# Optimization experiments

Hardware: AMD Instinct MI355X
Metric: run time of the kernel (lower is better)

Reference implementation:

```python
import jax, jax.numpy as jnp
import numpy as np

D_MODEL = 512
PROJ = 2 * D_MODEL  # 1024
N_STATES = 32
KSIZE = 4
LN_EPS = 1e-3  # keras LayerNormalization default epsilon


def setup_inputs() -> dict:
    key = jax.random.key(0)
    ks = jax.random.split(key, 16)
    B, L = 2, 2048
    s_in = 1.0 / np.sqrt(D_MODEL)
    s_pr = 1.0 / np.sqrt(PROJ)
    x = jax.random.normal(ks[0], (B, L, D_MODEL), dtype=jnp.float32)
    # LayerNorm params
    ln_gamma = jnp.ones((D_MODEL,), jnp.float32)
    ln_beta = jnp.zeros((D_MODEL,), jnp.float32)
    # dense1 / dense2: d_model -> proj
    W1 = jax.random.normal(ks[1], (D_MODEL, PROJ), jnp.float32) * s_in
    b1 = jnp.zeros((PROJ,), jnp.float32)
    W2 = jax.random.normal(ks[2], (D_MODEL, PROJ), jnp.float32) * s_in
    b2 = jnp.zeros((PROJ,), jnp.float32)
    # depthwise causal conv1d: kernel (K, 1, PROJ) in WIO layout, groups=PROJ
    conv_k = jax.random.normal(ks[3], (KSIZE, 1, PROJ), jnp.float32) * 0.5
    conv_b = jnp.zeros((PROJ,), jnp.float32)
    # SSM params
    A_log = jnp.log(jnp.broadcast_to(jnp.arange(1, N_STATES + 1, dtype=jnp.float32), (PROJ, N_STATES)))
    D_skip = jnp.ones((PROJ,), jnp.float32)
    WB = jax.random.normal(ks[4], (PROJ, N_STATES), jnp.float32) * s_pr
    bB = jnp.zeros((N_STATES,), jnp.float32)
    WC = jax.random.normal(ks[5], (PROJ, N_STATES), jnp.float32) * s_pr
    bC = jnp.zeros((N_STATES,), jnp.float32)
    Wd = jax.random.normal(ks[6], (PROJ, PROJ), jnp.float32) * s_pr
    bd = jnp.zeros((PROJ,), jnp.float32)
    # dense3: proj -> d_model
    W3 = jax.random.normal(ks[7], (PROJ, D_MODEL), jnp.float32) * s_pr
    b3 = jnp.zeros((D_MODEL,), jnp.float32)
    return dict(x=x, ln_gamma=ln_gamma, ln_beta=ln_beta, W1=W1, b1=b1, W2=W2, b2=b2,
                conv_k=conv_k, conv_b=conv_b, A_log=A_log, D_skip=D_skip,
                WB=WB, bB=bB, WC=WC, bC=bC, Wd=Wd, bd=bd, W3=W3, b3=b3)


def _layernorm(x, gamma, beta):
    mu = jnp.mean(x, axis=-1, keepdims=True)
    var = jnp.mean(jnp.square(x - mu), axis=-1, keepdims=True)
    return (x - mu) * jax.lax.rsqrt(var + LN_EPS) * gamma + beta


def _causal_dwconv(x, k, b):
    # x: [B,L,C], k: [K,1,C], depthwise causal conv (left-pad K-1)
    y = jax.lax.conv_general_dilated(
        x, k, window_strides=(1,), padding=[(KSIZE - 1, 0)],
        dimension_numbers=('NWC', 'WIO', 'NWC'), feature_group_count=PROJ)
    return y + b


def _selective_scan(u, delta, A, Bm, Cm, D_skip):
    # u, delta: [B,L,D]; A: [D,N]; Bm, Cm: [B,L,N]; D_skip: [D]
    deltaA = jnp.einsum('bld,dn->bldn', delta, A)                 # [B,L,D,N]
    deltaBu = jnp.einsum('bld,bld,bln->bldn', delta, u, Bm)        # [B,L,D,N]
    # shift deltaA left by one along L, zero at the end (pad trick in source)
    shifted = jnp.concatenate([deltaA[:, 1:], jnp.zeros_like(deltaA[:, :1])], axis=1)
    # reversed cumsum along L, then exp
    e = jnp.exp(jnp.flip(jnp.cumsum(jnp.flip(shifted, axis=1), axis=1), axis=1))
    xs = jnp.cumsum(deltaBu * e, axis=1) / (e + 1e-12)
    y = jnp.einsum('bldn,bln->bld', xs, Cm)
    return y + u * D_skip


def reference(x, ln_gamma, ln_beta, W1, b1, W2, b2, conv_k, conv_b,
              A_log, D_skip, WB, bB, WC, bC, Wd, bd, W3, b3):
    h = _layernorm(x, ln_gamma, ln_beta)
    x1 = h @ W1 + b1                      # [B,L,PROJ]
    x1 = _causal_dwconv(x1, conv_k, conv_b)
    x1 = jax.nn.silu(x1)
    A = -jnp.exp(A_log)                    # [PROJ,N]
    Cm = x1 @ WC + bC                      # [B,L,N]
    Bm = x1 @ WB + bB                      # [B,L,N]
    delta = jax.nn.softplus(x1 @ Wd + bd)  # [B,L,PROJ]
    y = _selective_scan(x1, delta, A, Bm, Cm, D_skip)
    x2 = jax.nn.silu(h @ W2 + b2)
    out = (y * x2) @ W3 + b3 + x           # residual; dropout is identity at inference
    return out
```

## Files before the change

kernel.cpp:

```cpp
#include <hip/hip_runtime.h>
#include <stdint.h>

#define L_SEQ 2048
#define BATCH 2
#define DMODEL 512
#define PROJ 1024
#define NST 32
#define NCATU 1088
#define ROWS (BATCH*L_SEQ)
#define THRESH 50.0f

typedef float f32x4 __attribute__((ext_vector_type(4)));
typedef short short8 __attribute__((ext_vector_type(8)));

__device__ inline float bf2f(unsigned short u){ uint32_t x=((uint32_t)u)<<16; float f; __builtin_memcpy(&f,&x,4); return f; }
__device__ inline unsigned short f2bf(float f){ uint32_t x; __builtin_memcpy(&x,&f,4); uint32_t r=x+0x7FFFu+((x>>16)&1u); return (unsigned short)(r>>16); }
__device__ inline float siluf(float x){ return x/(1.f+__expf(-x)); }
__device__ inline float softplusf(float x){ return x>20.f? x : log1pf(__expf(x)); }

#define AS1(p) ((const __attribute__((address_space(1))) void*)(p))
#define AS3(p) ((__attribute__((address_space(3))) void*)(p))

template<int N> __device__ inline void wait_vmcnt(){
  if constexpr (N==0)      asm volatile("s_waitcnt vmcnt(0)" ::: "memory");
  else if constexpr (N==2) asm volatile("s_waitcnt vmcnt(2)" ::: "memory");
  else if constexpr (N==4) asm volatile("s_waitcnt vmcnt(4)" ::: "memory");
  else if constexpr (N==6) asm volatile("s_waitcnt vmcnt(6)" ::: "memory");
  else                     asm volatile("s_waitcnt vmcnt(8)" ::: "memory");
}

__global__ __launch_bounds__(256)
void prep_kernel(const float* __restrict__ W1, const float* __restrict__ b1,
                 const float* __restrict__ W2, const float* __restrict__ b2,
                 const float* __restrict__ Wd, const float* __restrict__ bd,
                 const float* __restrict__ WB, const float* __restrict__ bB,
                 const float* __restrict__ WC, const float* __restrict__ bC,
                 const float* __restrict__ W3,
                 unsigned short* __restrict__ W12t, unsigned short* __restrict__ Wcatt,
                 unsigned short* __restrict__ W3t, float* __restrict__ bias12,
                 float* __restrict__ biascat)
{
  int i = blockIdx.x*256 + threadIdx.x;
  const int nA = 2048*512;
  const int nB = NCATU*1024;
  const int nC = 512*1024;
  if (i < nA) {
    int n = i >> 9, k = i & 511;
    float v = (n < 1024) ? W1[k*1024 + n] : W2[k*1024 + (n-1024)];
    W12t[i] = f2bf(v);
    return;
  }
  i -= nA;
  if (i < nB) {
    int n = i >> 10, k = i & 1023;
    float v;
    if (n < 1024) v = Wd[k*1024 + n];
    else if (n < 1056) v = WB[k*32 + (n-1024)];
    else v = WC[k*32 + (n-1056)];
    Wcatt[i] = f2bf(v);
    return;
  }
  i -= nB;
  if (i < nC) {
    int n = i >> 10, k = i & 1023;
    W3t[i] = f2bf(W3[k*512 + n]);
    return;
  }
  i -= nC;
  if (i < 2048) { bias12[i] = (i < 1024) ? b1[i] : b2[i-1024]; return; }
  i -= 2048;
  if (i < NCATU) {
    biascat[i] = (i < 1024) ? bd[i] : (i < 1056) ? bB[i-1024] : bC[i-1056];
  }
}

__global__ __launch_bounds__(256)
void ln_kernel(const float* __restrict__ x, const float* __restrict__ gamma,
               const float* __restrict__ beta, unsigned short* __restrict__ H)
{
  int row = blockIdx.x*4 + (threadIdx.x >> 6);
  int lane = threadIdx.x & 63;
  const float4* xr = (const float4*)(x + (size_t)row*DMODEL);
  float4 v0 = xr[lane];
  float4 v1 = xr[lane+64];
  float s = v0.x+v0.y+v0.z+v0.w + v1.x+v1.y+v1.z+v1.w;
  float q = v0.x*v0.x+v0.y*v0.y+v0.z*v0.z+v0.w*v0.w
          + v1.x*v1.x+v1.y*v1.y+v1.z*v1.z+v1.w*v1.w;
#pragma unroll
  for (int m=32;m>0;m>>=1){ s += __shfl_xor(s,m); q += __shfl_xor(q,m); }
  float mu = s*(1.f/DMODEL);
  float var = q*(1.f/DMODEL) - mu*mu;
  float rs = rsqrtf(var + 1e-3f);
  int c0 = lane*4, c1 = 256 + lane*4;
  float4 g0 = *(const float4*)&gamma[c0]; float4 g1 = *(const float4*)&gamma[c1];
  float4 t0 = *(const float4*)&beta[c0];  float4 t1 = *(const float4*)&beta[c1];
  ushort4 o0, o1;
  o0.x = f2bf((v0.x-mu)*rs*g0.x + t0.x);
  o0.y = f2bf((v0.y-mu)*rs*g0.y + t0.y);
  o0.z = f2bf((v0.z-mu)*rs*g0.z + t0.z);
  o0.w = f2bf((v0.w-mu)*rs*g0.w + t0.w);
  o1.x = f2bf((v1.x-mu)*rs*g1.x + t1.x);
  o1.y = f2bf((v1.y-mu)*rs*g1.y + t1.y);
  o1.z = f2bf((v1.z-mu)*rs*g1.z + t1.z);
  o1.w = f2bf((v1.w-mu)*rs*g1.w + t1.w);
  *(ushort4*)&H[(size_t)row*DMODEL + c0] = o0;
  *(ushort4*)&H[(size_t)row*DMODEL + c1] = o1;
}

template<int BM, int BN, int MODE>
__global__ __launch_bounds__(256)
void gemm_bt(const unsigned short* __restrict__ A, const unsigned short* __restrict__ Bt,
             void* __restrict__ Cv, const float* __restrict__ bias,
             const float* __restrict__ res, int M, int N, int K)
{
  constexpr int BK = 64;
  constexpr int AM = 2, AN = 2;
  constexpr int ASEGI = BM*BK/8/256;
  constexpr int BSEGI = BN*BK/8/256;
  constexpr int LPT = ASEGI + BSEGI;
  __shared__ unsigned short As[3][BM*BK];
  __shared__ unsigned short Bs[3][BN*BK];
  int tid = threadIdx.x;
  int lane = tid & 63, wid = tid >> 6;
  int wm = wid >> 1, wn = wid & 1;

  int gx = gridDim.x;
  int nwg = gx * gridDim.y;
  int L = blockIdx.y*gx + blockIdx.x;
  int W = (L & 7)*(nwg >> 3) + (L >> 3);
  int bx = W % gx, by = W / gx;
  int m0 = bx*BM, n0 = by*BN;

  f32x4 acc[AM][AN];
#pragma unroll
  for (int i=0;i<AM;i++)
#pragma unroll
    for (int j=0;j<AN;j++)
#pragma unroll
      for (int e=0;e<4;e++) acc[i][j][e] = 0.f;

  const unsigned short* ap[ASEGI];
  const unsigned short* bp[BSEGI];
#pragma unroll
  for (int j=0;j<ASEGI;j++){
    int s = tid + j*256;
    int row = s >> 3, kc = ((s & 7) ^ (row & 7)) * 8;
    ap[j] = A + (size_t)(m0+row)*K + kc;
  }
#pragma unroll
  for (int j=0;j<BSEGI;j++){
    int s = tid + j*256;
    int row = s >> 3, kc = ((s & 7) ^ (row & 7)) * 8;
    bp[j] = Bt + (size_t)(n0+row)*K + kc;
  }

  auto stage = [&](int buf){
#pragma unroll
    for (int j=0;j<ASEGI;j++){
      __builtin_amdgcn_global_load_lds(AS1(ap[j]), AS3(&As[buf][(size_t)(j*256 + wid*64)*8]), 16, 0, 0);
      ap[j] += BK;
    }
#pragma unroll
    for (int j=0;j<BSEGI;j++){
      __builtin_amdgcn_global_load_lds(AS1(bp[j]), AS3(&Bs[buf][(size_t)(j*256 + wid*64)*8]), 16, 0, 0);
      bp[j] += BK;
    }
  };

  stage(0);
  stage(1);
  int T = K/BK;
  int rb = 0, wb = 2;
  int r = lane & 15, kb = lane >> 4;
  for (int t = 0; t < T; ++t) {
    if (t+1 < T) wait_vmcnt<LPT>();
    else         wait_vmcnt<0>();
    __builtin_amdgcn_s_barrier();
    if (t+2 < T) { stage(wb); wb = (wb==2)?0:wb+1; }
#pragma unroll
    for (int ks=0; ks<2; ++ks) {
      short8 af[AM], bfr[AN];
#pragma unroll
      for (int i=0;i<AM;i++){
        int row = wm*32 + i*16 + r;
        int c = (ks*4 + kb) ^ (r & 7);
        af[i] = *(const short8*)&As[rb][(row*8 + c)*8];
      }
#pragma unroll
      for (int j=0;j<AN;j++){
        int row = wn*32 + j*16 + r;
        int c = (ks*4 + kb) ^ (r & 7);
        bfr[j] = *(const short8*)&Bs[rb][(row*8 + c)*8];
      }
#pragma unroll
      for (int i=0;i<AM;i++)
#pragma unroll
        for (int j=0;j<AN;j++)
          acc[i][j] = __builtin_amdgcn_mfma_f32_16x16x32_bf16(af[i], bfr[j], acc[i][j], 0,0,0);
    }
    rb = (rb==2)?0:rb+1;
  }

  int rr = (lane >> 4)*4, cc = lane & 15;
#pragma unroll
  for (int i=0;i<AM;i++)
#pragma unroll
    for (int j=0;j<AN;j++) {
      int col = n0 + wn*32 + j*16 + cc;
      float bcol = (MODE == 4) ? 0.f : bias[col];
#pragma unroll
      for (int e=0;e<4;e++) {
        int row = m0 + wm*32 + i*16 + rr + e;
        float v = acc[i][j][e];
        if constexpr (MODE == 4) {
          v += bias[row];
          if (row < 1024) v = softplusf(v);
          ((float*)Cv)[(size_t)row*N + col] = v;
        } else if constexpr (MODE == 0) {
          ((unsigned short*)Cv)[(size_t)row*N + col] = f2bf(v + bcol);
        } else {
          v += bcol + res[(size_t)row*N + col];
          ((float*)Cv)[(size_t)row*N + col] = v;
        }
      }
    }
}

__global__ __launch_bounds__(256)
void conv_silu_kernel(const unsigned short* __restrict__ P12, const float* __restrict__ ck,
                      const float* __restrict__ cb, unsigned short* __restrict__ ubf,
                      unsigned short* __restrict__ x2bf)
{
  int gid = blockIdx.x*256 + threadIdx.x;
  int c4 = gid & 511;
  int row = gid >> 9;
  int l = row & (L_SEQ-1);
  if (c4 < 256) {
    int c = c4*4;
    float4 bv = *(const float4*)&cb[c];
    float r0=bv.x, r1=bv.y, r2=bv.z, r3=bv.w;
#pragma unroll
    for (int t=0;t<4;t++){
      int lsrc = l - 3 + t;
      if (lsrc >= 0) {
        ushort4 xv = *(const ushort4*)&P12[(size_t)(row-3+t)*2048 + c];
        float4 kv = *(const float4*)&ck[t*PROJ + c];
        r0 = fmaf(bf2f(xv.x),kv.x,r0);
        r1 = fmaf(bf2f(xv.y),kv.y,r1);
        r2 = fmaf(bf2f(xv.z),kv.z,r2);
        r3 = fmaf(bf2f(xv.w),kv.w,r3);
      }
    }
    ushort4 o;
    o.x=f2bf(siluf(r0)); o.y=f2bf(siluf(r1)); o.z=f2bf(siluf(r2)); o.w=f2bf(siluf(r3));
    *(ushort4*)&ubf[(size_t)row*PROJ + c] = o;
  } else {
    int c = (c4-256)*4;
    ushort4 xv = *(const ushort4*)&P12[(size_t)row*2048 + 1024 + c];
    ushort4 o;
    o.x=f2bf(siluf(bf2f(xv.x))); o.y=f2bf(siluf(bf2f(xv.y)));
    o.z=f2bf(siluf(bf2f(xv.z))); o.w=f2bf(siluf(bf2f(xv.w)));
    *(ushort4*)&x2bf[(size_t)row*PROJ + c] = o;
  }
}

__global__ __launch_bounds__(256)
void tsum_kernel(const float* __restrict__ CT, float* __restrict__ suf8,
                 int* __restrict__ l0out)
{
  int G = blockIdx.x;
  int b = G >> 10, d = G & 1023;
  const float* row = CT + (size_t)d*ROWS + b*L_SEQ;
  int t = threadIdx.x;
  float4 v0 = *(const float4*)&row[t*8];
  float4 v1 = *(const float4*)&row[t*8+4];
  float vals[8] = {v0.x,v0.y,v0.z,v0.w,v1.x,v1.y,v1.z,v1.w};
  float part = 0.f;
#pragma unroll
  for (int i=0;i<8;i++) part += vals[i];
  __shared__ float ps[256];
  ps[t] = part; __syncthreads();
  for (int off=1; off<256; off<<=1){
    float v = (t >= off) ? ps[t-off] : 0.f;
    __syncthreads();
    ps[t] += v;
    __syncthreads();
  }
  float T = ps[255];
  float prefx = ps[t] - part;
  suf8[(size_t)G*(L_SEQ/8) + t] = T - prefx;
  float run = prefx; int cnt = 0;
#pragma unroll
  for (int i=0;i<8;i++){
    float suf_l = T - run;
    cnt += (suf_l >= THRESH) ? 1 : 0;
    run += vals[i];
  }
  __shared__ int cs[256];
  cs[t] = cnt; __syncthreads();
  for (int off=128; off>0; off>>=1){ if (t < off) cs[t] += cs[t+off]; __syncthreads(); }
  if (t == 0) {
    int total = cs[0];
    l0out[G] = total > 0 ? total-1 : 0;
  }
}

__global__ __launch_bounds__(256)
void scan_kernel(const float* __restrict__ CT, const float* __restrict__ suf8,
                 const unsigned short* __restrict__ ubf, const float* __restrict__ A_log,
                 const int* __restrict__ l0arr, float* __restrict__ ystate)
{
  int tid = threadIdx.x;
  int n = tid & 31;
  int G = blockIdx.x*8 + (tid >> 5);
  int b = G >> 10, d = G & 1023;
  float np1 = __expf(A_log[d*NST + n]);
  int myl0 = l0arr[G];
  int base = min(myl0, __shfl_xor(myl0, 32)) & ~7;
  const float* dT = CT + (size_t)d*ROWS + b*L_SEQ;
  const float* Br = CT + (size_t)(1024+n)*ROWS + b*L_SEQ;
  const float* Cr = CT + (size_t)(1056+n)*ROWS + b*L_SEQ;
  const float* s8 = suf8 + (size_t)G*(L_SEQ/8);
  const unsigned short* ub = ubf + (size_t)b*L_SEQ*PROJ + d;
  float* yb = ystate + (size_t)b*L_SEQ*PROJ + d;
  float s = 0.f;
  for (int l = base; l < L_SEQ; l += 8) {
    float4 d0 = *(const float4*)&dT[l];
    float4 d1 = *(const float4*)&dT[l+4];
    float4 B0 = *(const float4*)&Br[l];
    float4 B1 = *(const float4*)&Br[l+4];
    float4 C0 = *(const float4*)&Cr[l];
    float4 C1 = *(const float4*)&Cr[l+4];
    float sufv = s8[l >> 3];
    float dl[8] = {d0.x,d0.y,d0.z,d0.w,d1.x,d1.y,d1.z,d1.w};
    float Bv[8] = {B0.x,B0.y,B0.z,B0.w,B1.x,B1.y,B1.z,B1.w};
    float Cv[8] = {C0.x,C0.y,C0.z,C0.w,C1.x,C1.y,C1.z,C1.w};
    float uu[8];
#pragma unroll
    for (int t=0;t<8;t++) uu[t] = bf2f(ub[(size_t)(l+t)*PROJ]);
    float cum = 0.f;
#pragma unroll
    for (int t=0;t<8;t++){
      cum += dl[t];
      float decay = __expf(-dl[t]*np1);
      s = fmaf(decay, s, dl[t]*uu[t]*Bv[t]);
      float gte = 1.f/(1.f + 1e-12f*__expf(np1*(sufv - cum)));
      float contrib = s*gte*Cv[t];
#pragma unroll
      for (int m=16;m>0;m>>=1) contrib += __shfl_xor(contrib, m);
      if (n == 0) yb[(size_t)(l+t)*PROJ] = contrib;
    }
  }
}

__global__ __launch_bounds__(256)
void zmul_kernel(const float* __restrict__ ystate, const unsigned short* __restrict__ ubf,
                 const unsigned short* __restrict__ x2bf, const float* __restrict__ Dskip,
                 const int* __restrict__ l0arr, unsigned short* __restrict__ zbf)
{
  size_t i = ((size_t)blockIdx.x*256 + threadIdx.x)*4;
  int d = (int)(i & (PROJ-1));
  int row = (int)(i >> 10);
  int l = row & (L_SEQ-1);
  int b = row >> 11;
  int4 l0v = *(const int4*)&l0arr[b*PROJ + d];
  float4 ys = *(const float4*)&ystate[i];
  ys.x = (l >= l0v.x) ? ys.x : 0.f;
  ys.y = (l >= l0v.y) ? ys.y : 0.f;
  ys.z = (l >= l0v.z) ? ys.z : 0.f;
  ys.w = (l >= l0v.w) ? ys.w : 0.f;
  ushort4 uu = *(const ushort4*)&ubf[i];
  ushort4 xx = *(const ushort4*)&x2bf[i];
  float4 Dv = *(const float4*)&Dskip[d];
  ushort4 o;
  o.x = f2bf((ys.x + bf2f(uu.x)*Dv.x)*bf2f(xx.x));
  o.y = f2bf((ys.y + bf2f(uu.y)*Dv.y)*bf2f(xx.y));
  o.z = f2bf((ys.z + bf2f(uu.z)*Dv.z)*bf2f(xx.z));
  o.w = f2bf((ys.w + bf2f(uu.w)*Dv.w)*bf2f(xx.w));
  *(ushort4*)&zbf[i] = o;
}

extern "C" void kernel_launch(void* const* d_in, const int* in_sizes, int n_in,
                              void* d_out, int out_size, void* d_ws, size_t ws_size,
                              hipStream_t stream)
{
  const float* x     = (const float*)d_in[0];
  const float* ln_g  = (const float*)d_in[1];
  const float* ln_b  = (const float*)d_in[2];
  const float* W1    = (const float*)d_in[3];
  const float* b1    = (const float*)d_in[4];
  const float* W2    = (const float*)d_in[5];
  const float* b2    = (const float*)d_in[6];
  const float* convk = (const float*)d_in[7];
  const float* convb = (const float*)d_in[8];
  const float* A_log = (const float*)d_in[9];
  const float* Dskip = (const float*)d_in[10];
  const float* WB    = (const float*)d_in[11];
  const float* bB    = (const float*)d_in[12];
  const float* WC    = (const float*)d_in[13];
  const float* bC    = (const float*)d_in[14];
  const float* Wd    = (const float*)d_in[15];
  const float* bd    = (const float*)d_in[16];
  const float* W3    = (const float*)d_in[17];
  const float* b3    = (const float*)d_in[18];

  char* w = (char*)d_ws;
  auto alloc = [&](size_t bytes){ char* p = w; w += (bytes + 255) & ~(size_t)255; return p; };
  unsigned short* Hbf    = (unsigned short*)alloc((size_t)ROWS*DMODEL*2);
  unsigned short* W12t   = (unsigned short*)alloc((size_t)2048*512*2);
  unsigned short* Wcatt  = (unsigned short*)alloc((size_t)NCATU*1024*2);
  unsigned short* W3t    = (unsigned short*)alloc((size_t)512*1024*2);
  float*          bias12 = (float*)alloc(2048*4);
  float*          biascat= (float*)alloc(NCATU*4);
  unsigned short* P12    = (unsigned short*)alloc((size_t)ROWS*2048*2);
  unsigned short* ubf    = (unsigned short*)alloc((size_t)ROWS*PROJ*2);
  unsigned short* x2bf   = (unsigned short*)alloc((size_t)ROWS*PROJ*2);
  float*          CT     = (float*)alloc((size_t)NCATU*ROWS*4);
  float*          suf8   = (float*)alloc((size_t)2048*(L_SEQ/8)*4);
  int*            l0arr  = (int*)alloc(2048*4);
  float*          ystate = (float*)alloc((size_t)ROWS*PROJ*4);
  unsigned short* zbf    = (unsigned short*)alloc((size_t)ROWS*PROJ*2);

  {
    int total = 2048*512 + NCATU*1024 + 512*1024 + 2048 + NCATU;
    prep_kernel<<<(total+255)/256, 256, 0, stream>>>(W1,b1,W2,b2,Wd,bd,WB,bB,WC,bC,W3,
                                                     W12t,Wcatt,W3t,bias12,biascat);
  }
  ln_kernel<<<ROWS/4, 256, 0, stream>>>(x, ln_g, ln_b, Hbf);

  dim3 g1(ROWS/64, 2048/64);
  gemm_bt<64,64,0><<<g1, 256, 0, stream>>>(Hbf, W12t, P12, bias12, nullptr, ROWS, 2048, DMODEL);

  conv_silu_kernel<<<ROWS*512/256, 256, 0, stream>>>(P12, convk, convb, ubf, x2bf);

  dim3 g2(NCATU/64, ROWS/64);
  gemm_bt<64,64,4><<<g2, 256, 0, stream>>>(Wcatt, ubf, CT, biascat, nullptr, NCATU, ROWS, PROJ);

  tsum_kernel<<<2048, 256, 0, stream>>>(CT, suf8, l0arr);

  scan_kernel<<<2048/8, 256, 0, stream>>>(CT, suf8, ubf, A_log, l0arr, ystate);

  zmul_kernel<<<(ROWS*PROJ/4)/256, 256, 0, stream>>>(ystate, ubf, x2bf, Dskip, l0arr, zbf);

  dim3 g3(ROWS/64, DMODEL/64);
  gemm_bt<64,64,3><<<g3, 256, 0, stream>>>(zbf, W3t, (float*)d_out, b3, x, ROWS, DMODEL, PROJ);
}
```

Baseline: 160.2 us.

## Replace tiled GEMM with weight-stationary GEMM keeping weights in registers

Replaces the generic 64x64 LDS-tiled GEMM with a weight-stationary kernel. Each wave keeps its 16 weight columns over the full K dimension in registers, and only activation tiles are streamed through a triple-buffered LDS pipeline, with each block handling two 64-token tiles. The aim is to drop the weight-tile LDS staging and halve the LDS reads per MFMA. The cost is heavy register use (up to 128 VGPRs for K=1024), lower occupancy, and fewer blocks for the output projection.

```diff
diff --git a/kernel.cpp b/kernel.cpp
--- a/kernel.cpp
+++ b/kernel.cpp
@@ -24,9 +24,7 @@
 template<int N> __device__ inline void wait_vmcnt(){
   if constexpr (N==0)      asm volatile("s_waitcnt vmcnt(0)" ::: "memory");
   else if constexpr (N==2) asm volatile("s_waitcnt vmcnt(2)" ::: "memory");
-  else if constexpr (N==4) asm volatile("s_waitcnt vmcnt(4)" ::: "memory");
-  else if constexpr (N==6) asm volatile("s_waitcnt vmcnt(6)" ::: "memory");
-  else                     asm volatile("s_waitcnt vmcnt(8)" ::: "memory");
+  else                     asm volatile("s_waitcnt vmcnt(4)" ::: "memory");
 }
 
 __global__ __launch_bounds__(256)
@@ -107,123 +105,98 @@
   *(ushort4*)&H[(size_t)row*DMODEL + c1] = o1;
 }
 
-template<int BM, int BN, int MODE>
-__global__ __launch_bounds__(256)
-void gemm_bt(const unsigned short* __restrict__ A, const unsigned short* __restrict__ Bt,
-             void* __restrict__ Cv, const float* __restrict__ bias,
-             const float* __restrict__ res, int M, int N, int K)
-{
-  constexpr int BK = 64;
-  constexpr int AM = 2, AN = 2;
-  constexpr int ASEGI = BM*BK/8/256;
-  constexpr int BSEGI = BN*BK/8/256;
-  constexpr int LPT = ASEGI + BSEGI;
-  __shared__ unsigned short As[3][BM*BK];
-  __shared__ unsigned short Bs[3][BN*BK];
+template<int KD, int TT, int MODE>
+__global__ __launch_bounds__(256)
+void wgemm(const unsigned short* __restrict__ W, const unsigned short* __restrict__ Act,
+           void* __restrict__ out, const float* __restrict__ bias,
+           const float* __restrict__ res)
+{
+  constexpr int T = KD/64;
+  __shared__ unsigned short As[3][64*64];
   int tid = threadIdx.x;
   int lane = tid & 63, wid = tid >> 6;
-  int wm = wid >> 1, wn = wid & 1;
-
-  int gx = gridDim.x;
-  int nwg = gx * gridDim.y;
-  int L = blockIdx.y*gx + blockIdx.x;
-  int W = (L & 7)*(nwg >> 3) + (L >> 3);
-  int bx = W % gx, by = W / gx;
-  int m0 = bx*BM, n0 = by*BN;
-
-  f32x4 acc[AM][AN];
-#pragma unroll
-  for (int i=0;i<AM;i++)
-#pragma unroll
-    for (int j=0;j<AN;j++)
-#pragma unroll
-      for (int e=0;e<4;e++) acc[i][j][e] = 0.f;
-
-  const unsigned short* ap[ASEGI];
-  const unsigned short* bp[BSEGI];
-#pragma unroll
-  for (int j=0;j<ASEGI;j++){
-    int s = tid + j*256;
-    int row = s >> 3, kc = ((s & 7) ^ (row & 7)) * 8;
-    ap[j] = A + (size_t)(m0+row)*K + kc;
-  }
-#pragma unroll
-  for (int j=0;j<BSEGI;j++){
-    int s = tid + j*256;
-    int row = s >> 3, kc = ((s & 7) ^ (row & 7)) * 8;
-    bp[j] = Bt + (size_t)(n0+row)*K + kc;
-  }
-
-  auto stage = [&](int buf){
-#pragma unroll
-    for (int j=0;j<ASEGI;j++){
-      __builtin_amdgcn_global_load_lds(AS1(ap[j]), AS3(&As[buf][(size_t)(j*256 + wid*64)*8]), 16, 0, 0);
-      ap[j] += BK;
+  int r = lane & 15, kb = lane >> 4;
+  int c = blockIdx.x*64 + wid*16 + r;
+
+  short8 breg[KD/32];
+#pragma unroll
+  for (int kc=0; kc<KD/32; ++kc)
+    breg[kc] = *(const short8*)&W[(size_t)c*KD + kc*32 + kb*8];
+
+  for (int tt=0; tt<TT; ++tt) {
+    int tok0 = (blockIdx.y*TT + tt)*64;
+    const unsigned short* ap[2];
+#pragma unroll
+    for (int j=0;j<2;j++){
+      int s = tid + j*256;
+      int row = s >> 3, kc = ((s & 7) ^ (row & 7)) * 8;
+      ap[j] = Act + (size_t)(tok0+row)*KD + kc;
     }
-#pragma unroll
-    for (int j=0;j<BSEGI;j++){
-      __builtin_amdgcn_global_load_lds(AS1(bp[j]), AS3(&Bs[buf][(size_t)(j*256 + wid*64)*8]), 16, 0, 0);
-      bp[j] += BK;
-    }
-  };
-
-  stage(0);
-  stage(1);
-  int T = K/BK;
-  int rb = 0, wb = 2;
-  int r = lane & 15, kb = lane >> 4;
-  for (int t = 0; t < T; ++t) {
-    if (t+1 < T) wait_vmcnt<LPT>();
-    else         wait_vmcnt<0>();
-    __builtin_amdgcn_s_barrier();
-    if (t+2 < T) { stage(wb); wb = (wb==2)?0:wb+1; }
-#pragma unroll
-    for (int ks=0; ks<2; ++ks) {
-      short8 af[AM], bfr[AN];
-#pragma unroll
-      for (int i=0;i<AM;i++){
-        int row = wm*32 + i*16 + r;
-        int c = (ks*4 + kb) ^ (r & 7);
-        af[i] = *(const short8*)&As[rb][(row*8 + c)*8];
+    auto stage = [&](int buf){
+#pragma unroll
+      for (int j=0;j<2;j++){
+        __builtin_amdgcn_global_load_lds(AS1(ap[j]), AS3(&As[buf][(size_t)(j*256 + wid*64)*8]), 16, 0, 0);
+        ap[j] += 64;
       }
-#pragma unroll
-      for (int j=0;j<AN;j++){
-        int row = wn*32 + j*16 + r;
-        int c = (ks*4 + kb) ^ (r & 7);
-        bfr[j] = *(const short8*)&Bs[rb][(row*8 + c)*8];
-      }
-#pragma unroll
-      for (int i=0;i<AM;i++)
-#pragma unroll
-        for (int j=0;j<AN;j++)
-          acc[i][j] = __builtin_amdgcn_mfma_f32_16x16x32_bf16(af[i], bfr[j], acc[i][j], 0,0,0);
-    }
-    rb = (rb==2)?0:rb+1;
-  }
-
-  int rr = (lane >> 4)*4, cc = lane & 15;
-#pragma unroll
-  for (int i=0;i<AM;i++)
-#pragma unroll
-    for (int j=0;j<AN;j++) {
-      int col = n0 + wn*32 + j*16 + cc;
-      float bcol = (MODE == 4) ? 0.f : bias[col];
-#pragma unroll
-      for (int e=0;e<4;e++) {
-        int row = m0 + wm*32 + i*16 + rr + e;
-        float v = acc[i][j][e];
-        if constexpr (MODE == 4) {
-          v += bias[row];
-          if (row < 1024) v = softplusf(v);
-          ((float*)Cv)[(size_t)row*N + col] = v;
-        } else if constexpr (MODE == 0) {
-          ((unsigned short*)Cv)[(size_t)row*N + col] = f2bf(v + bcol);
-        } else {
-          v += bcol + res[(size_t)row*N + col];
-          ((float*)Cv)[(size_t)row*N + col] = v;
+    };
+    stage(0);
+    if (T > 1) stage(1);
+
+    f32x4 acc[4];
+#pragma unroll
+    for (int i=0;i<4;i++)
+#pragma unroll
+      for (int e=0;e<4;e++) acc[i][e] = 0.f;
+
+#pragma unroll
+    for (int t=0; t<T; ++t) {
+      if (t+1 < T) wait_vmcnt<2>();
+      else         wait_vmcnt<0>();
+      __builtin_amdgcn_s_barrier();
+      if (t+2 < T) stage((t+2)%3);
+#pragma unroll
+      for (int ks=0; ks<2; ++ks) {
+        short8 af[4];
+#pragma unroll
+        for (int i=0;i<4;i++){
+          int row = i*16 + r;
+          int cx = (ks*4 + kb) ^ (r & 7);
+          af[i] = *(const short8*)&As[t%3][(row*8 + cx)*8];
         }
+#pragma unroll
+        for (int i=0;i<4;i++)
+          acc[i] = __builtin_amdgcn_mfma_f32_16x16x32_bf16(af[i], breg[t*2+ks], acc[i], 0,0,0);
       }
     }
+
+    int rr = kb*4;
+    float bv = bias[c];
+    if constexpr (MODE == 1) {
+#pragma unroll
+      for (int i=0;i<4;i++)
+#pragma unroll
+        for (int e=0;e<4;e++)
+          ((unsigned short*)out)[(size_t)(tok0 + i*16 + rr + e)*2048 + c] = f2bf(acc[i][e] + bv);
+    } else if constexpr (MODE == 2) {
+#pragma unroll
+      for (int i=0;i<4;i++){
+        float4 o;
+        float v0 = acc[i][0] + bv, v1 = acc[i][1] + bv, v2 = acc[i][2] + bv, v3 = acc[i][3] + bv;
+        if (c < 1024) { v0 = softplusf(v0); v1 = softplusf(v1); v2 = softplusf(v2); v3 = softplusf(v3); }
+        o.x = v0; o.y = v1; o.z = v2; o.w = v3;
+        *(float4*)&((float*)out)[(size_t)c*ROWS + tok0 + i*16 + rr] = o;
+      }
+    } else {
+#pragma unroll
+      for (int i=0;i<4;i++)
+#pragma unroll
+        for (int e=0;e<4;e++){
+          int row = tok0 + i*16 + rr + e;
+          ((float*)out)[(size_t)row*512 + c] = acc[i][e] + bv + res[(size_t)row*512 + c];
+        }
+    }
+    __syncthreads();
+  }
 }
 
 __global__ __launch_bounds__(256)
@@ -428,13 +401,11 @@
   }
   ln_kernel<<<ROWS/4, 256, 0, stream>>>(x, ln_g, ln_b, Hbf);
 
-  dim3 g1(ROWS/64, 2048/64);
-  gemm_bt<64,64,0><<<g1, 256, 0, stream>>>(Hbf, W12t, P12, bias12, nullptr, ROWS, 2048, DMODEL);
+  wgemm<512,2,1><<<dim3(2048/64, 32), 256, 0, stream>>>(W12t, Hbf, P12, bias12, nullptr);
 
   conv_silu_kernel<<<ROWS*512/256, 256, 0, stream>>>(P12, convk, convb, ubf, x2bf);
 
-  dim3 g2(NCATU/64, ROWS/64);
-  gemm_bt<64,64,4><<<g2, 256, 0, stream>>>(Wcatt, ubf, CT, biascat, nullptr, NCATU, ROWS, PROJ);
+  wgemm<1024,2,2><<<dim3(NCATU/64, 32), 256, 0, stream>>>(Wcatt, ubf, CT, biascat, nullptr);
 
   tsum_kernel<<<2048, 256, 0, stream>>>(CT, suf8, l0arr);
 
@@ -442,6 +413,5 @@
 
   zmul_kernel<<<(ROWS*PROJ/4)/256, 256, 0, stream>>>(ystate, ubf, x2bf, Dskip, l0arr, zbf);
 
-  dim3 g3(ROWS/64, DMODEL/64);
-  gemm_bt<64,64,3><<<g3, 256, 0, stream>>>(zbf, W3t, (float*)d_out, b3, x, ROWS, DMODEL, PROJ);
-}
+  wgemm<1024,2,3><<<dim3(512/64, 32), 256, 0, stream>>>(W3t, zbf, (float*)d_out, b3, x);
+}
```

Result: slower. 163.5 us (+2.1%).
